# Kernel optimization log

Hardware: AMD Instinct MI355X
Metric: run time of the kernel (lower is better)

The kernel has to match this reference:

```python
import jax, jax.numpy as jnp
import numpy as np

NUM_HEADS = 16
TOP_K = 128
LN_EPS = 1e-5


def layernorm(x, w, b):
    mu = jnp.mean(x, axis=-1, keepdims=True)
    var = jnp.mean((x - mu) ** 2, axis=-1, keepdims=True)
    return (x - mu) * jax.lax.rsqrt(var + LN_EPS) * w + b


def top_k_activation(x, k):
    # keep top-k along last dim, zero elsewhere (scatter, like torch.scatter_)
    n = x.shape[-1]
    if k >= n:
        return x
    vals, idx = jax.lax.top_k(x, k)
    flat = x.reshape(-1, n)
    rows = jnp.arange(flat.shape[0])[:, None]
    out = jnp.zeros_like(flat).at[rows, idx.reshape(-1, k)].set(vals.reshape(-1, k))
    return out.reshape(x.shape)


def setup_inputs() -> dict:
    key = jax.random.key(0)
    ks = jax.random.split(key, 8)
    B, S, H = 2, 2048, 1024
    hd = H // NUM_HEADS
    return {
        "x": jax.random.normal(ks[0], (B, S, H), dtype=jnp.float32),
        "W_Q": jax.random.normal(ks[1], (H, H), dtype=jnp.float32) * 0.02,
        "W_K": jax.random.normal(ks[2], (H, H), dtype=jnp.float32) * 0.02,
        "W_V": jax.random.normal(ks[3], (H, H), dtype=jnp.float32) * 0.02,
        "W_O": jax.random.normal(ks[4], (H, H), dtype=jnp.float32) * 0.02,
        "q_ln_w": jnp.ones((hd,), dtype=jnp.float32),
        "q_ln_b": jnp.zeros((hd,), dtype=jnp.float32),
        "k_ln_w": jnp.ones((hd,), dtype=jnp.float32),
        "k_ln_b": jnp.zeros((hd,), dtype=jnp.float32),
        "sparse_W_V": jax.random.normal(ks[5], (NUM_HEADS, hd, TOP_K), dtype=jnp.float32) * 0.02,
        "sparse_W_O": jax.random.normal(ks[6], (NUM_HEADS, TOP_K, hd), dtype=jnp.float32) * 0.02,
    }


def reference(x, W_Q, W_K, W_V, W_O, q_ln_w, q_ln_b, k_ln_w, k_ln_b, sparse_W_V, sparse_W_O):
    B, S, H = x.shape
    nh = sparse_W_V.shape[0]
    hd = H // nh
    # projections (torch Linear: x @ W.T)
    def split_heads(t):
        return t.reshape(B, S, nh, hd).transpose(0, 2, 1, 3)  # [B, nh, S, hd]
    Q = split_heads(jnp.einsum('bsd,od->bso', x, W_Q))
    K = split_heads(jnp.einsum('bsd,od->bso', x, W_K))
    V = split_heads(jnp.einsum('bsd,od->bso', x, W_V))
    Q = layernorm(Q, q_ln_w, q_ln_b)
    K = layernorm(K, k_ln_w, k_ln_b)
    scores = jnp.einsum('bhqd,bhkd->bhqk', Q, K) / jnp.sqrt(jnp.float32(hd))
    attn = jax.nn.softmax(scores, axis=-1)
    context = jnp.einsum('bhqk,bhkd->bhqd', attn, V)  # [B, nh, S, hd]
    # faithful to source: transpose then reshape mixes batch/seq/head dims
    context_flat = context.transpose(0, 2, 1, 3).reshape(B * nh, S, hd)
    v_weights = sparse_W_V.mean(axis=2)  # [nh, hd]
    z = jnp.einsum('bnd,hd->bhn', context_flat, v_weights)  # [B*nh, nh, S]
    z_sparse = top_k_activation(z, TOP_K)  # top-k along seq axis, as in source
    o_weights = sparse_W_O.mean(axis=1)  # [nh, hd]
    y_flat = jnp.einsum('bhn,hd->bnd', z_sparse, o_weights)  # [B*nh, S, hd]
    y = y_flat.reshape(B, nh, S, hd).transpose(0, 2, 1, 3).reshape(B, S, H)
    y = jnp.einsum('bsd,od->bso', y, W_O)
    return y
```

## Files before the change

kernel.cpp:

```cpp
#include <hip/hip_runtime.h>
#include <math.h>

#define NB   2
#define SEQ  2048
#define NHD  16
#define HDD  64
#define HID  1024
#define TOPK 128

__global__ void k_prep_means(const float* __restrict__ sWV, const float* __restrict__ sWO,
                             double* __restrict__ vw, double* __restrict__ ow) {
  int t = threadIdx.x;
  for (int o = t; o < NHD * HDD; o += 256) {
    const float* p = sWV + (size_t)o * TOPK;
    double s = 0.0;
    for (int i = 0; i < TOPK; i++) s += (double)p[i];
    vw[o] = s * (1.0 / 128.0);
    int h = o >> 6, d = o & 63;
    const float* q = sWO + ((size_t)h * TOPK) * HDD + d;
    double s2 = 0.0;
    for (int i = 0; i < TOPK; i++) s2 += (double)q[(size_t)i * HDD];
    ow[o] = s2 * (1.0 / 128.0);
  }
}

__global__ void k_prep_wvp_g(const float* __restrict__ W_V, const float* __restrict__ W_O,
                             const double* __restrict__ vw, const double* __restrict__ ow,
                             double* __restrict__ WVP, float* __restrict__ G) {
  int blk = blockIdx.x;
  int t = threadIdx.x;
  if (blk < 256) {
    int n = blk >> 4, h = blk & 15;
    for (int j = t; j < HID; j += 256) {
      double s = 0.0;
      for (int d = 0; d < 64; d++)
        s += (double)W_V[(size_t)(n * 64 + d) * HID + j] * vw[h * 64 + d];
      WVP[(size_t)blk * HID + j] = s;
    }
  } else {
    int r = blk - 256;
    int m = r >> 4, h = r & 15;
    for (int o = t; o < HID; o += 256) {
      double s = 0.0;
      for (int d = 0; d < 64; d++)
        s += ow[h * 64 + d] * (double)W_O[(size_t)o * HID + m * 64 + d];
      G[(size_t)r * HID + o] = (float)s;
    }
  }
}

__global__ __launch_bounds__(256) void k_proj_qk(
    const float* __restrict__ x, const float* __restrict__ W_Q, const float* __restrict__ W_K,
    const float* __restrict__ qw, const float* __restrict__ qb,
    const float* __restrict__ kw, const float* __restrict__ kb,
    double* __restrict__ Qh, double* __restrict__ Kh) {
  __shared__ float  As[64][33];
  __shared__ float  Bs[64][33];
  __shared__ double Cs[64][65];
  __shared__ double red[64][4];

  int rt = blockIdx.x, ot = blockIdx.y;
  bool isQ = (ot < 16);
  const float* W = isQ ? W_Q : W_K;
  int head = isQ ? ot : ot - 16;
  int o0 = head * 64;
  int t = threadIdx.x;
  int tr = t >> 4, tc = t & 15;

  double acc[4][4];
  #pragma unroll
  for (int i = 0; i < 4; i++)
    #pragma unroll
    for (int j = 0; j < 4; j++) acc[i][j] = 0.0;

  for (int k0 = 0; k0 < HID; k0 += 32) {
    #pragma unroll
    for (int i = 0; i < 8; i++) {
      int idx = t + i * 256;
      int r = idx >> 5, c = idx & 31;
      As[r][c] = x[(size_t)(rt * 64 + r) * HID + k0 + c];
      Bs[r][c] = W[(size_t)(o0 + r) * HID + k0 + c];
    }
    __syncthreads();
    #pragma unroll 1
    for (int kk = 0; kk < 32; kk++) {
      double a[4], b[4];
      #pragma unroll
      for (int i = 0; i < 4; i++) a[i] = (double)As[tr * 4 + i][kk];
      #pragma unroll
      for (int j = 0; j < 4; j++) b[j] = (double)Bs[tc * 4 + j][kk];
      #pragma unroll
      for (int i = 0; i < 4; i++)
        #pragma unroll
        for (int j = 0; j < 4; j++) acc[i][j] = fma(a[i], b[j], acc[i][j]);
    }
    __syncthreads();
  }

  #pragma unroll
  for (int i = 0; i < 4; i++)
    #pragma unroll
    for (int j = 0; j < 4; j++) Cs[tr * 4 + i][tc * 4 + j] = acc[i][j];
  __syncthreads();

  int r = t >> 2, p = t & 3;
  double s = 0.0;
  for (int i = 0; i < 16; i++) s += Cs[r][p * 16 + i];
  red[r][p] = s;
  __syncthreads();
  double mu = (red[r][0] + red[r][1] + red[r][2] + red[r][3]) * (1.0 / 64.0);
  __syncthreads();
  double s2 = 0.0;
  for (int i = 0; i < 16; i++) { double dl = Cs[r][p * 16 + i] - mu; s2 += dl * dl; }
  red[r][p] = s2;
  __syncthreads();
  double var = (red[r][0] + red[r][1] + red[r][2] + red[r][3]) * (1.0 / 64.0);
  double inv = 1.0 / sqrt(var + 1e-5);

  int R = rt * 64 + r;
  int b = R >> 11, ss = R & 2047;
  const float* lw = isQ ? qw : kw;
  const float* lb = isQ ? qb : kb;
  double* outp = isQ ? Qh : Kh;
  size_t base = (((size_t)b * 16 + head) * SEQ + ss) * 64;
  for (int i = 0; i < 16; i++) {
    int d = p * 16 + i;
    outp[base + d] = (Cs[r][d] - mu) * inv * (double)lw[d] + (double)lb[d];
  }
}

__global__ __launch_bounds__(256) void k_proj_vp(
    const float* __restrict__ x, const double* __restrict__ WVP, double* __restrict__ Vp) {
  __shared__ float  As[64][33];
  __shared__ double Bs[64][33];
  int rt = blockIdx.x, ot = blockIdx.y;
  int t = threadIdx.x, tr = t >> 4, tc = t & 15;

  double acc[4][4];
  #pragma unroll
  for (int i = 0; i < 4; i++)
    #pragma unroll
    for (int j = 0; j < 4; j++) acc[i][j] = 0.0;

  for (int k0 = 0; k0 < HID; k0 += 32) {
    #pragma unroll
    for (int i = 0; i < 8; i++) {
      int idx = t + i * 256;
      int r = idx >> 5, c = idx & 31;
      As[r][c] = x[(size_t)(rt * 64 + r) * HID + k0 + c];
      Bs[r][c] = WVP[(size_t)(ot * 64 + r) * HID + k0 + c];
    }
    __syncthreads();
    #pragma unroll 1
    for (int kk = 0; kk < 32; kk++) {
      double a[4], b[4];
      #pragma unroll
      for (int i = 0; i < 4; i++) a[i] = (double)As[tr * 4 + i][kk];
      #pragma unroll
      for (int j = 0; j < 4; j++) b[j] = Bs[tc * 4 + j][kk];
      #pragma unroll
      for (int i = 0; i < 4; i++)
        #pragma unroll
        for (int j = 0; j < 4; j++) acc[i][j] = fma(a[i], b[j], acc[i][j]);
    }
    __syncthreads();
  }
  #pragma unroll
  for (int i = 0; i < 4; i++) {
    int R = rt * 64 + tr * 4 + i;
    int b = R >> 11, k = R & 2047;
    #pragma unroll
    for (int j = 0; j < 4; j++) {
      int cc = ot * 64 + tc * 4 + j;
      int n = cc >> 4, h = cc & 15;
      Vp[((((size_t)b * 16 + n) * SEQ) + k) * 16 + h] = acc[i][j];
    }
  }
}

__global__ __launch_bounds__(256, 2) void k_attn(
    const double* __restrict__ Qh, const double* __restrict__ Kh,
    const double* __restrict__ Vp, double* __restrict__ pnum, double* __restrict__ pden) {
  int kh = blockIdx.x;
  int qt = blockIdx.y;
  int bn = blockIdx.z;
  int t = threadIdx.x;
  int s = qt * 256 + t;

  __shared__ double Klds[64][64];
  __shared__ double Vplds[64][16];

  double qd[64];
  const double* qp = Qh + ((size_t)bn * SEQ + s) * 64;
  #pragma unroll
  for (int d = 0; d < 64; d++) qd[d] = qp[d];

  double num[16];
  #pragma unroll
  for (int h = 0; h < 16; h++) num[h] = 0.0;
  double den = 0.0;

  int k0 = kh * 1024;
  for (int kc = 0; kc < 1024; kc += 64) {
    const double* kbase = Kh + ((size_t)bn * SEQ + k0 + kc) * 64;
    #pragma unroll
    for (int i = 0; i < 16; i++) {
      int idx = t + i * 256;
      Klds[idx >> 6][idx & 63] = kbase[idx];
    }
    const double* vbase = Vp + ((size_t)bn * SEQ + k0 + kc) * 16;
    #pragma unroll
    for (int i = 0; i < 4; i++) {
      int idx = t + i * 256;
      Vplds[idx >> 4][idx & 15] = vbase[idx];
    }
    __syncthreads();
    #pragma unroll 1
    for (int kk = 0; kk < 64; kk += 4) {
      double s0 = 0.0, s1 = 0.0, s2 = 0.0, s3 = 0.0;
      #pragma unroll
      for (int d = 0; d < 64; d++) {
        double q = qd[d];
        s0 = fma(q, Klds[kk + 0][d], s0);
        s1 = fma(q, Klds[kk + 1][d], s1);
        s2 = fma(q, Klds[kk + 2][d], s2);
        s3 = fma(q, Klds[kk + 3][d], s3);
      }
      double e0 = exp(s0 * 0.125);
      double e1 = exp(s1 * 0.125);
      double e2 = exp(s2 * 0.125);
      double e3 = exp(s3 * 0.125);
      den += (e0 + e1) + (e2 + e3);
      #pragma unroll
      for (int h = 0; h < 16; h++) {
        double a = num[h];
        a = fma(e0, Vplds[kk + 0][h], a);
        a = fma(e1, Vplds[kk + 1][h], a);
        a = fma(e2, Vplds[kk + 2][h], a);
        a = fma(e3, Vplds[kk + 3][h], a);
        num[h] = a;
      }
    }
    __syncthreads();
  }
  size_t pb = ((size_t)kh * 32 + bn) * SEQ + s;
  pden[pb] = den;
  #pragma unroll
  for (int h = 0; h < 16; h++) pnum[pb * 16 + h] = num[h];
}

__global__ void k_combine(const double* __restrict__ pnum, const double* __restrict__ pden,
                          double* __restrict__ zrow) {
  int id = blockIdx.x * 256 + threadIdx.x;
  int bn = id >> 11, s = id & 2047;
  int b = bn >> 4, n = bn & 15;
  double den = pden[id] + pden[65536 + id];
  int bp = b * 16 + (s >> 7);
  int np = ((s & 127) << 4) | n;
  size_t p0 = (size_t)id * 16, p1 = ((size_t)65536 + id) * 16;
  for (int h = 0; h < 16; h++) {
    double nm = pnum[p0 + h] + pnum[p1 + h];
    zrow[((size_t)bp * 16 + h) * 2048 + np] = nm / den;
  }
}

__device__ inline unsigned long long dkey(double v) {
  unsigned long long u = (unsigned long long)__double_as_longlong(v);
  return (u & 0x8000000000000000ULL) ? ~u : (u | 0x8000000000000000ULL);
}

__global__ __launch_bounds__(256) void k_topk(const double* __restrict__ zrow,
                                              float* __restrict__ zs) {
  int row = blockIdx.x;
  int t = threadIdx.x;
  const double* src = zrow + (size_t)row * 2048;
  double v[8];
  unsigned long long key[8];
  #pragma unroll
  for (int i = 0; i < 8; i++) { v[i] = src[t + i * 256]; key[i] = dkey(v[i]); }

  __shared__ unsigned sh_cnt[4];
  __shared__ unsigned sh_cg[4], sh_ce[4];
  int w = t >> 6, lane = t & 63;

  unsigned long long lo = 0ULL, hi = 0xFFFFFFFFFFFFFFFFULL;
  while (lo < hi) {
    unsigned long long mid = lo + ((hi - lo) >> 1);
    unsigned c = 0;
    #pragma unroll
    for (int i = 0; i < 8; i++) c += (key[i] > mid) ? 1u : 0u;
    for (int off = 32; off; off >>= 1) c += __shfl_down(c, off);
    if (lane == 0) sh_cnt[w] = c;
    __syncthreads();
    unsigned total = sh_cnt[0] + sh_cnt[1] + sh_cnt[2] + sh_cnt[3];
    __syncthreads();
    if (total < TOPK) hi = mid; else lo = mid + 1;
  }
  unsigned long long tau = lo;

  unsigned cg = 0, ce = 0;
  #pragma unroll
  for (int i = 0; i < 8; i++) {
    cg += (key[i] > tau) ? 1u : 0u;
    ce += (key[i] == tau) ? 1u : 0u;
  }
  for (int off = 32; off; off >>= 1) { cg += __shfl_down(cg, off); ce += __shfl_down(ce, off); }
  if (lane == 0) { sh_cg[w] = cg; sh_ce[w] = ce; }
  __syncthreads();
  unsigned c_gt = sh_cg[0] + sh_cg[1] + sh_cg[2] + sh_cg[3];
  unsigned c_eq = sh_ce[0] + sh_ce[1] + sh_ce[2] + sh_ce[3];
  unsigned need = TOPK - c_gt;

  unsigned idxThr = 2048;
  if (c_eq > need) {
    unsigned l2 = 0, h2 = 2048;
    while (l2 < h2) {
      unsigned m2 = (l2 + h2) >> 1;
      unsigned c = 0;
      #pragma unroll
      for (int i = 0; i < 8; i++) {
        unsigned idx = (unsigned)(t + i * 256);
        c += (key[i] == tau && idx < m2) ? 1u : 0u;
      }
      for (int off = 32; off; off >>= 1) c += __shfl_down(c, off);
      if (lane == 0) sh_cnt[w] = c;
      __syncthreads();
      unsigned tot = sh_cnt[0] + sh_cnt[1] + sh_cnt[2] + sh_cnt[3];
      __syncthreads();
      if (tot >= need) h2 = m2; else l2 = m2 + 1;
    }
    idxThr = l2;
  }

  float* dst = zs + (size_t)row * 2048;
  #pragma unroll
  for (int i = 0; i < 8; i++) {
    unsigned idx = (unsigned)(t + i * 256);
    bool keep = (key[i] > tau) ||
                (key[i] == tau && (c_eq <= need || idx < idxThr));
    dst[idx] = keep ? (float)v[i] : 0.0f;
  }
}

__global__ __launch_bounds__(256) void k_out(const float* __restrict__ zs,
                                             const float* __restrict__ G,
                                             float* __restrict__ out) {
  __shared__ float Al[64][65];
  __shared__ float Bl[64][65];
  int rt = blockIdx.x, ot = blockIdx.y;
  int t = threadIdx.x, tr = t >> 4, tc = t & 15;
  int Rb = rt * 64;
  int b = Rb >> 11, s0 = Rb & 2047;

  float acc[4][4];
  #pragma unroll
  for (int i = 0; i < 4; i++)
    #pragma unroll
    for (int j = 0; j < 4; j++) acc[i][j] = 0.0f;

  for (int kc = 0; kc < 256; kc += 64) {
    #pragma unroll
    for (int i = 0; i < 16; i++) {
      int idx = t + i * 256;
      int c = idx >> 6, r = idx & 63;
      int cc = kc + c;
      Al[r][c] = zs[(((size_t)(b * 16 + (cc >> 4))) * 16 + (cc & 15)) * 2048 + s0 + r];
      Bl[c][r] = G[(size_t)(kc + c) * HID + ot * 64 + r];
    }
    __syncthreads();
    #pragma unroll 1
    for (int kk = 0; kk < 64; kk++) {
      float a[4], bb[4];
      #pragma unroll
      for (int i = 0; i < 4; i++) a[i] = Al[tr * 4 + i][kk];
      #pragma unroll
      for (int j = 0; j < 4; j++) bb[j] = Bl[kk][tc * 4 + j];
      #pragma unroll
      for (int i = 0; i < 4; i++)
        #pragma unroll
        for (int j = 0; j < 4; j++) acc[i][j] = fmaf(a[i], bb[j], acc[i][j]);
    }
    __syncthreads();
  }
  #pragma unroll
  for (int i = 0; i < 4; i++) {
    int R = Rb + tr * 4 + i;
    #pragma unroll
    for (int j = 0; j < 4; j++)
      out[(size_t)R * HID + ot * 64 + tc * 4 + j] = acc[i][j];
  }
}

extern "C" void kernel_launch(void* const* d_in, const int* in_sizes, int n_in,
                              void* d_out, int out_size, void* d_ws, size_t ws_size,
                              hipStream_t stream) {
  const float* x   = (const float*)d_in[0];
  const float* W_Q = (const float*)d_in[1];
  const float* W_K = (const float*)d_in[2];
  const float* W_V = (const float*)d_in[3];
  const float* W_O = (const float*)d_in[4];
  const float* qw  = (const float*)d_in[5];
  const float* qb  = (const float*)d_in[6];
  const float* kw  = (const float*)d_in[7];
  const float* kb  = (const float*)d_in[8];
  const float* sWV = (const float*)d_in[9];
  const float* sWO = (const float*)d_in[10];
  float* out = (float*)d_out;
  char* ws = (char*)d_ws;

  double* Qh   = (double*)(ws + 0);
  double* Kh   = (double*)(ws + 33554432ULL);
  double* Vp   = (double*)(ws + 67108864ULL);
  double* WVP  = (double*)(ws + 75497472ULL);
  float*  G    = (float*) (ws + 77594624ULL);
  double* vw   = (double*)(ws + 78643200ULL);
  double* ow   = (double*)(ws + 78651392ULL);
  double* pnum = (double*)(ws + 78659584ULL);
  double* pden = (double*)(ws + 95436800ULL);
  double* zrow = (double*)(ws + 0);
  float*  zs   = (float*) (ws + 8388608ULL);

  k_prep_means<<<dim3(1), dim3(256), 0, stream>>>(sWV, sWO, vw, ow);
  k_prep_wvp_g<<<dim3(512), dim3(256), 0, stream>>>(W_V, W_O, vw, ow, WVP, G);
  k_proj_qk<<<dim3(64, 32), dim3(256), 0, stream>>>(x, W_Q, W_K, qw, qb, kw, kb, Qh, Kh);
  k_proj_vp<<<dim3(64, 4), dim3(256), 0, stream>>>(x, WVP, Vp);
  k_attn<<<dim3(2, 8, 32), dim3(256), 0, stream>>>(Qh, Kh, Vp, pnum, pden);
  k_combine<<<dim3(256), dim3(256), 0, stream>>>(pnum, pden, zrow);
  k_topk<<<dim3(512), dim3(256), 0, stream>>>(zrow, zs);
  k_out<<<dim3(64, 16), dim3(256), 0, stream>>>(zs, G, out);
}
```

Measured before the change: 1.624 ms.

## Split attention head dim across thread pairs and transpose GEMM smem tiles

The attention kernel now assigns each query to two threads, each owning half of the 64-wide head dimension and half of the 16 output columns. Partial scores are combined with lane shuffles and the exp work is divided between the pair. This cuts per-thread registers, since the old design held 64 doubles of Q plus 16 accumulators, and doubles the grid for better occupancy, at the cost of extra shuffles. Separately, the projection GEMMs store shared-memory tiles transposed so each thread reads its four operands with one vector load instead of four strided scalar loads.

Result: slower. 2.092 ms (+28.8%).

```diff
diff --git a/kernel.cpp b/kernel.cpp
--- a/kernel.cpp
+++ b/kernel.cpp
@@ -54,8 +54,8 @@
     const float* __restrict__ qw, const float* __restrict__ qb,
     const float* __restrict__ kw, const float* __restrict__ kb,
     double* __restrict__ Qh, double* __restrict__ Kh) {
-  __shared__ float  As[64][33];
-  __shared__ float  Bs[64][33];
+  __shared__ float  AsT[32][68];
+  __shared__ float  BsT[32][68];
   __shared__ double Cs[64][65];
   __shared__ double red[64][4];
 
@@ -78,17 +78,17 @@
     for (int i = 0; i < 8; i++) {
       int idx = t + i * 256;
       int r = idx >> 5, c = idx & 31;
-      As[r][c] = x[(size_t)(rt * 64 + r) * HID + k0 + c];
-      Bs[r][c] = W[(size_t)(o0 + r) * HID + k0 + c];
+      AsT[c][r] = x[(size_t)(rt * 64 + r) * HID + k0 + c];
+      BsT[c][r] = W[(size_t)(o0 + r) * HID + k0 + c];
     }
     __syncthreads();
     #pragma unroll 1
     for (int kk = 0; kk < 32; kk++) {
+      float4 af = *(const float4*)&AsT[kk][tr * 4];
+      float4 bf = *(const float4*)&BsT[kk][tc * 4];
       double a[4], b[4];
-      #pragma unroll
-      for (int i = 0; i < 4; i++) a[i] = (double)As[tr * 4 + i][kk];
-      #pragma unroll
-      for (int j = 0; j < 4; j++) b[j] = (double)Bs[tc * 4 + j][kk];
+      a[0] = (double)af.x; a[1] = (double)af.y; a[2] = (double)af.z; a[3] = (double)af.w;
+      b[0] = (double)bf.x; b[1] = (double)bf.y; b[2] = (double)bf.z; b[3] = (double)bf.w;
       #pragma unroll
       for (int i = 0; i < 4; i++)
         #pragma unroll
@@ -131,8 +131,8 @@
 
 __global__ __launch_bounds__(256) void k_proj_vp(
     const float* __restrict__ x, const double* __restrict__ WVP, double* __restrict__ Vp) {
-  __shared__ float  As[64][33];
-  __shared__ double Bs[64][33];
+  __shared__ float  AsT[32][68];
+  __shared__ double BsT[32][68];
   int rt = blockIdx.x, ot = blockIdx.y;
   int t = threadIdx.x, tr = t >> 4, tc = t & 15;
 
@@ -147,17 +147,18 @@
     for (int i = 0; i < 8; i++) {
       int idx = t + i * 256;
       int r = idx >> 5, c = idx & 31;
-      As[r][c] = x[(size_t)(rt * 64 + r) * HID + k0 + c];
-      Bs[r][c] = WVP[(size_t)(ot * 64 + r) * HID + k0 + c];
+      AsT[c][r] = x[(size_t)(rt * 64 + r) * HID + k0 + c];
+      BsT[c][r] = WVP[(size_t)(ot * 64 + r) * HID + k0 + c];
     }
     __syncthreads();
     #pragma unroll 1
     for (int kk = 0; kk < 32; kk++) {
+      float4 af = *(const float4*)&AsT[kk][tr * 4];
+      double2 b01 = *(const double2*)&BsT[kk][tc * 4];
+      double2 b23 = *(const double2*)&BsT[kk][tc * 4 + 2];
       double a[4], b[4];
-      #pragma unroll
-      for (int i = 0; i < 4; i++) a[i] = (double)As[tr * 4 + i][kk];
-      #pragma unroll
-      for (int j = 0; j < 4; j++) b[j] = Bs[tc * 4 + j][kk];
+      a[0] = (double)af.x; a[1] = (double)af.y; a[2] = (double)af.z; a[3] = (double)af.w;
+      b[0] = b01.x; b[1] = b01.y; b[2] = b23.x; b[3] = b23.y;
       #pragma unroll
       for (int i = 0; i < 4; i++)
         #pragma unroll
@@ -178,75 +179,95 @@
   }
 }
 
-__global__ __launch_bounds__(256, 2) void k_attn(
+__global__ __launch_bounds__(256) void k_attn(
     const double* __restrict__ Qh, const double* __restrict__ Kh,
     const double* __restrict__ Vp, double* __restrict__ pnum, double* __restrict__ pden) {
   int kh = blockIdx.x;
   int qt = blockIdx.y;
   int bn = blockIdx.z;
   int t = threadIdx.x;
-  int s = qt * 256 + t;
-
-  __shared__ double Klds[64][64];
-  __shared__ double Vplds[64][16];
-
-  double qd[64];
-  const double* qp = Qh + ((size_t)bn * SEQ + s) * 64;
-  #pragma unroll
-  for (int d = 0; d < 64; d++) qd[d] = qp[d];
-
-  double num[16];
-  #pragma unroll
-  for (int h = 0; h < 16; h++) num[h] = 0.0;
+  int dh = t & 1;
+  int s = qt * 128 + (t >> 1);
+
+  __shared__ double2 K2[64][32];
+  __shared__ double2 V2[64][8];
+
+  double2 q2[16];
+  const double2* qp = (const double2*)(Qh + ((size_t)bn * SEQ + s) * 64 + dh * 32);
+  #pragma unroll
+  for (int i = 0; i < 16; i++) q2[i] = qp[i];
+
+  double2 num2[4];
+  #pragma unroll
+  for (int i = 0; i < 4; i++) { num2[i].x = 0.0; num2[i].y = 0.0; }
   double den = 0.0;
 
   int k0 = kh * 1024;
   for (int kc = 0; kc < 1024; kc += 64) {
-    const double* kbase = Kh + ((size_t)bn * SEQ + k0 + kc) * 64;
-    #pragma unroll
-    for (int i = 0; i < 16; i++) {
+    const double2* kb = (const double2*)(Kh + ((size_t)bn * SEQ + k0 + kc) * 64);
+    #pragma unroll
+    for (int i = 0; i < 8; i++) {
       int idx = t + i * 256;
-      Klds[idx >> 6][idx & 63] = kbase[idx];
-    }
-    const double* vbase = Vp + ((size_t)bn * SEQ + k0 + kc) * 16;
-    #pragma unroll
-    for (int i = 0; i < 4; i++) {
+      K2[idx >> 5][idx & 31] = kb[idx];
+    }
+    const double2* vb = (const double2*)(Vp + ((size_t)bn * SEQ + k0 + kc) * 16);
+    #pragma unroll
+    for (int i = 0; i < 2; i++) {
       int idx = t + i * 256;
-      Vplds[idx >> 4][idx & 15] = vbase[idx];
+      V2[idx >> 3][idx & 7] = vb[idx];
     }
     __syncthreads();
     #pragma unroll 1
     for (int kk = 0; kk < 64; kk += 4) {
       double s0 = 0.0, s1 = 0.0, s2 = 0.0, s3 = 0.0;
       #pragma unroll
-      for (int d = 0; d < 64; d++) {
-        double q = qd[d];
-        s0 = fma(q, Klds[kk + 0][d], s0);
-        s1 = fma(q, Klds[kk + 1][d], s1);
-        s2 = fma(q, Klds[kk + 2][d], s2);
-        s3 = fma(q, Klds[kk + 3][d], s3);
+      for (int d2 = 0; d2 < 16; d2++) {
+        double2 qq = q2[d2];
+        double2 k0v = K2[kk + 0][dh * 16 + d2];
+        double2 k1v = K2[kk + 1][dh * 16 + d2];
+        double2 k2v = K2[kk + 2][dh * 16 + d2];
+        double2 k3v = K2[kk + 3][dh * 16 + d2];
+        s0 = fma(qq.x, k0v.x, s0); s0 = fma(qq.y, k0v.y, s0);
+        s1 = fma(qq.x, k1v.x, s1); s1 = fma(qq.y, k1v.y, s1);
+        s2 = fma(qq.x, k2v.x, s2); s2 = fma(qq.y, k2v.y, s2);
+        s3 = fma(qq.x, k3v.x, s3); s3 = fma(qq.y, k3v.y, s3);
       }
-      double e0 = exp(s0 * 0.125);
-      double e1 = exp(s1 * 0.125);
-      double e2 = exp(s2 * 0.125);
-      double e3 = exp(s3 * 0.125);
+      s0 += __shfl_xor(s0, 1); s1 += __shfl_xor(s1, 1);
+      s2 += __shfl_xor(s2, 1); s3 += __shfl_xor(s3, 1);
+      double xa = dh ? s2 : s0;
+      double xb = dh ? s3 : s1;
+      double ea = exp(xa * 0.125);
+      double eb = exp(xb * 0.125);
+      double pa = __shfl_xor(ea, 1);
+      double pb = __shfl_xor(eb, 1);
+      double e0 = dh ? pa : ea;
+      double e1 = dh ? pb : eb;
+      double e2 = dh ? ea : pa;
+      double e3 = dh ? eb : pb;
       den += (e0 + e1) + (e2 + e3);
       #pragma unroll
-      for (int h = 0; h < 16; h++) {
-        double a = num[h];
-        a = fma(e0, Vplds[kk + 0][h], a);
-        a = fma(e1, Vplds[kk + 1][h], a);
-        a = fma(e2, Vplds[kk + 2][h], a);
-        a = fma(e3, Vplds[kk + 3][h], a);
-        num[h] = a;
+      for (int h2 = 0; h2 < 4; h2++) {
+        double2 v0 = V2[kk + 0][dh * 4 + h2];
+        double2 v1 = V2[kk + 1][dh * 4 + h2];
+        double2 v2 = V2[kk + 2][dh * 4 + h2];
+        double2 v3 = V2[kk + 3][dh * 4 + h2];
+        double2 a = num2[h2];
+        a.x = fma(e0, v0.x, a.x); a.x = fma(e1, v1.x, a.x);
+        a.x = fma(e2, v2.x, a.x); a.x = fma(e3, v3.x, a.x);
+        a.y = fma(e0, v0.y, a.y); a.y = fma(e1, v1.y, a.y);
+        a.y = fma(e2, v2.y, a.y); a.y = fma(e3, v3.y, a.y);
+        num2[h2] = a;
       }
     }
     __syncthreads();
   }
-  size_t pb = ((size_t)kh * 32 + bn) * SEQ + s;
-  pden[pb] = den;
-  #pragma unroll
-  for (int h = 0; h < 16; h++) pnum[pb * 16 + h] = num[h];
+  size_t pb_ = ((size_t)kh * 32 + bn) * SEQ + s;
+  if (dh == 0) pden[pb_] = den;
+  #pragma unroll
+  for (int h2 = 0; h2 < 4; h2++) {
+    pnum[pb_ * 16 + dh * 8 + 2 * h2]     = num2[h2].x;
+    pnum[pb_ * 16 + dh * 8 + 2 * h2 + 1] = num2[h2].y;
+  }
 }
 
 __global__ void k_combine(const double* __restrict__ pnum, const double* __restrict__ pden,
@@ -424,7 +445,7 @@
   k_prep_wvp_g<<<dim3(512), dim3(256), 0, stream>>>(W_V, W_O, vw, ow, WVP, G);
   k_proj_qk<<<dim3(64, 32), dim3(256), 0, stream>>>(x, W_Q, W_K, qw, qb, kw, kb, Qh, Kh);
   k_proj_vp<<<dim3(64, 4), dim3(256), 0, stream>>>(x, WVP, Vp);
-  k_attn<<<dim3(2, 8, 32), dim3(256), 0, stream>>>(Qh, Kh, Vp, pnum, pden);
+  k_attn<<<dim3(2, 16, 32), dim3(256), 0, stream>>>(Qh, Kh, Vp, pnum, pden);
   k_combine<<<dim3(256), dim3(256), 0, stream>>>(pnum, pden, zrow);
   k_topk<<<dim3(512), dim3(256), 0, stream>>>(zrow, zs);
   k_out<<<dim3(64, 16), dim3(256), 0, stream>>>(zs, G, out);
```
